# Kernel optimization log

Hardware: AMD Instinct MI355X
Metric: run time of the kernel (lower is better)

The kernel has to match this reference:

```python
import jax, jax.numpy as jnp
import numpy as np

B, S, D, H = 4, 2048, 1024, 16
HD = D // H
FF = 4 * D
EPS = 1e-5


def _layer_norm(x, w, b):
    mu = jnp.mean(x, axis=-1, keepdims=True)
    var = jnp.mean(jnp.square(x - mu), axis=-1, keepdims=True)
    return (x - mu) * jax.lax.rsqrt(var + EPS) * w + b


def setup_inputs() -> dict:
    key = jax.random.key(0)
    ks = jax.random.split(key, 8)
    std = 0.02
    return {
        "x": jax.random.normal(ks[0], (B, S, D), dtype=jnp.float32),
        "ln1_w": jnp.ones((D,), jnp.float32),
        "ln1_b": jnp.zeros((D,), jnp.float32),
        "w_qkv": jax.random.normal(ks[1], (D, 3 * D), dtype=jnp.float32) * std,  # fused QKV, no bias
        "w_proj": jax.random.normal(ks[2], (D, D), dtype=jnp.float32) * std,
        "b_proj": jnp.zeros((D,), jnp.float32),
        "ln2_w": jnp.ones((D,), jnp.float32),
        "ln2_b": jnp.zeros((D,), jnp.float32),
        "w_ff1": jax.random.normal(ks[3], (D, FF), dtype=jnp.float32) * std,
        "b_ff1": jnp.zeros((FF,), jnp.float32),
        "w_ff2": jax.random.normal(ks[4], (FF, D), dtype=jnp.float32) * std,
        "b_ff2": jnp.zeros((D,), jnp.float32),
    }


def reference(x, ln1_w, ln1_b, w_qkv, w_proj, b_proj, ln2_w, ln2_b, w_ff1, b_ff1, w_ff2, b_ff2):
    b, s, d = x.shape
    # --- attention branch (pre-LN) ---
    h = _layer_norm(x, ln1_w, ln1_b)
    kqv = (h @ w_qkv).reshape(b, s, H, HD, 3)  # fused projection, split by last index
    k, q, v = kqv[..., 0], kqv[..., 1], kqv[..., 2]  # each [b, s, H, HD]
    scores = jnp.einsum("bqhd,bkhd->bhqk", q, k) * (HD ** -0.5)  # [b,H,s,s]
    causal = jnp.tril(jnp.ones((s, s), dtype=bool))
    scores = jnp.where(causal, scores, -jnp.inf)
    weights = jax.nn.softmax(scores, axis=-1)
    ctx = jnp.einsum("bhqk,bkhd->bqhd", weights, v).reshape(b, s, d)
    attn_out = ctx @ w_proj + b_proj
    x = x + attn_out
    # --- feed-forward branch (pre-LN) ---
    h = _layer_norm(x, ln2_w, ln2_b)
    ff = jax.nn.gelu(h @ w_ff1 + b_ff1, approximate=False) @ w_ff2 + b_ff2
    return x + ff
```

## Files before the change

kernel.cpp:

```cpp
#include <hip/hip_runtime.h>

typedef unsigned short u16;
typedef unsigned int u32;
typedef __bf16 bf16x8 __attribute__((ext_vector_type(8)));
typedef float f32x4 __attribute__((ext_vector_type(4)));
typedef float f32x16 __attribute__((ext_vector_type(16)));
typedef unsigned short us8 __attribute__((ext_vector_type(8)));
typedef unsigned short us4 __attribute__((ext_vector_type(4)));
typedef unsigned int u32x4 __attribute__((ext_vector_type(4)));

#define B_ 4
#define S_ 2048
#define D_ 1024
#define H_ 16
#define HD_ 64
#define EPS_ 1e-5f
#define SCALE_ (0.125f * 1.44269504088896341f)
#define THR_ 3.0f

__device__ __forceinline__ u16 f2bf(float f) {
  unsigned u = __builtin_bit_cast(unsigned, f);
  u = (u + 0x7FFFu + ((u >> 16) & 1u)) >> 16;
  return (u16)u;
}

__device__ __forceinline__ float gelu_f(float x) {
  float u = x * (2.3022388f + 0.10294971f * x * x);
  float te = __builtin_amdgcn_exp2f(u);
  return x - x * __builtin_amdgcn_rcpf(1.0f + te);
}

typedef const __attribute__((address_space(1))) unsigned int* gp1;
typedef __attribute__((address_space(3))) unsigned int* lp3;
__device__ __forceinline__ void gl_lds16(const void* g, void* l) {
  __builtin_amdgcn_global_load_lds((gp1)(unsigned long long)g,
                                   (lp3)(unsigned int)(unsigned long long)l,
                                   16, 0, 0);
}

__device__ __forceinline__ u32 cvtpk_bf16(float lo, float hi) {
  u32 d;
  asm("v_cvt_pk_bf16_f32 %0, %1, %2" : "=v"(d) : "v"(lo), "v"(hi));
  return d;
}
__device__ __forceinline__ void swap32(u32& a, u32& b) {
  asm("v_permlane32_swap_b32 %0, %1" : "+v"(a), "+v"(b));
}

__device__ __forceinline__ f32x16 zero16() {
  f32x16 z;
#pragma unroll
  for (int i = 0; i < 16; i++) z[i] = 0.f;
  return z;
}

__global__ __launch_bounds__(256) void wconv_kernel(const float* __restrict__ W,
                                                    u16* __restrict__ Wt,
                                                    int Kd, int N) {
  __shared__ u16 tile[32][33];
  int bid = blockIdx.x;
  int nbn = N >> 5;
  int tk = bid / nbn, tn = bid % nbn;
  int tx = threadIdx.x & 31, ty = threadIdx.x >> 5;
#pragma unroll
  for (int i = 0; i < 4; i++) {
    int r = ty + i * 8;
    tile[r][tx] = f2bf(W[(size_t)(tk * 32 + r) * N + tn * 32 + tx]);
  }
  __syncthreads();
#pragma unroll
  for (int i = 0; i < 4; i++) {
    int r = ty + i * 8;
    Wt[(size_t)(tn * 32 + r) * Kd + tk * 32 + tx] = tile[tx][r];
  }
}

__global__ __launch_bounds__(256) void vtrans_kernel(const u16* __restrict__ Vc,
                                                     u16* __restrict__ Vt) {
  __shared__ u16 tile[64][72];
  int bh = blockIdx.x >> 5;
  int sb = blockIdx.x & 31;
  const u16* src = Vc + ((size_t)bh * S_ + sb * 64) * HD_;
  int r = threadIdx.x >> 2, c0 = (threadIdx.x & 3) * 16;
  *(us8*)&tile[r][c0] = *(const us8*)(src + r * HD_ + c0);
  *(us8*)&tile[r][c0 + 8] = *(const us8*)(src + r * HD_ + c0 + 8);
  __syncthreads();
  u16* dst = Vt + (size_t)bh * HD_ * S_ + sb * 64;
  int hd = threadIdx.x >> 2;
  int s0 = (threadIdx.x & 3) * 16;
  us8 a, b;
#pragma unroll
  for (int j = 0; j < 8; j++) a[j] = tile[s0 + j][hd];
#pragma unroll
  for (int j = 0; j < 8; j++) b[j] = tile[s0 + 8 + j][hd];
  *(us8*)(dst + (size_t)hd * S_ + s0) = a;
  *(us8*)(dst + (size_t)hd * S_ + s0 + 8) = b;
}

__global__ __launch_bounds__(256) void ln_kernel(const float* __restrict__ x,
                                                 const float* __restrict__ w,
                                                 const float* __restrict__ b,
                                                 u16* __restrict__ out) {
  int row = blockIdx.x;
  int t = threadIdx.x;
  int lane = t & 63, wid = t >> 6;
  const float4* xr = (const float4*)(x + (size_t)row * D_);
  float4 v = xr[t];
  float s = v.x + v.y + v.z + v.w;
  float q = v.x * v.x + v.y * v.y + v.z * v.z + v.w * v.w;
#pragma unroll
  for (int off = 1; off < 64; off <<= 1) {
    s += __shfl_xor(s, off);
    q += __shfl_xor(q, off);
  }
  __shared__ float red[8];
  if (lane == 0) { red[wid] = s; red[4 + wid] = q; }
  __syncthreads();
  s = red[0] + red[1] + red[2] + red[3];
  q = red[4] + red[5] + red[6] + red[7];
  float mu = s * (1.0f / D_);
  float var = q * (1.0f / D_) - mu * mu;
  float rs = rsqrtf(var + EPS_);
  int c = t * 4;
  float4 wv = *(const float4*)(w + c);
  float4 bv = *(const float4*)(b + c);
  us4 o;
  o[0] = f2bf((v.x - mu) * rs * wv.x + bv.x);
  o[1] = f2bf((v.y - mu) * rs * wv.y + bv.y);
  o[2] = f2bf((v.z - mu) * rs * wv.z + bv.z);
  o[3] = f2bf((v.w - mu) * rs * wv.w + bv.w);
  *(us4*)(out + (size_t)row * D_ + c) = o;
}

template <int MODE>
__global__ __launch_bounds__(256, 3) void gemm_kernel(
    const u16* __restrict__ A, const u16* __restrict__ Bt,
    const float* __restrict__ bias, const float* __restrict__ res,
    float* __restrict__ Cf, u16* __restrict__ Cb,
    u16* __restrict__ Qc, u16* __restrict__ Kc, u16* __restrict__ Vc,
    int M, int N, int K) {
  __shared__ __align__(16) u16 Al[2][128 * 32];
  __shared__ __align__(16) u16 Bl[2][128 * 32];
  int t = threadIdx.x;
  int nbn = N >> 7;
  int nwg = gridDim.x;
  int cpx = nwg >> 3;
  int bid = (blockIdx.x % 8) * cpx + blockIdx.x / 8;
  int bm = bid / nbn, bn = bid % nbn;
  int lane = t & 63, wid = t >> 6;
  int wm = wid >> 1, wn = wid & 1;
  int lrow = lane & 15, lgr = lane >> 4;
  const u16* Ab = A + (size_t)bm * 128 * K;
  const u16* Bb = Bt + (size_t)bn * 128 * K;
  int srow = t >> 2;
  int sslot = (t & 3) ^ (srow & 3);
  const u16* Asrc = Ab + (size_t)srow * K + sslot * 8;
  const u16* Bsrc = Bb + (size_t)srow * K + sslot * 8;
  int rdslot = lgr ^ (lrow & 3);

  f32x4 acc[4][4] = {};
  int NT = K >> 5;
  {
    gl_lds16(Asrc, &Al[0][t * 8]);
    gl_lds16(Asrc + (size_t)64 * K, &Al[0][2048 + t * 8]);
    gl_lds16(Bsrc, &Bl[0][t * 8]);
    gl_lds16(Bsrc + (size_t)64 * K, &Bl[0][2048 + t * 8]);
  }
  for (int kt = 0; kt < NT; kt++) {
    int cur = kt & 1;
    if (kt + 1 < NT) {
      int k1 = (kt + 1) * 32;
      u16* Ad = &Al[cur ^ 1][t * 8];
      u16* Bd = &Bl[cur ^ 1][t * 8];
      gl_lds16(Asrc + k1, Ad);
      gl_lds16(Asrc + (size_t)64 * K + k1, Ad + 2048);
      gl_lds16(Bsrc + k1, Bd);
      gl_lds16(Bsrc + (size_t)64 * K + k1, Bd + 2048);
      asm volatile("s_waitcnt vmcnt(4)" ::: "memory");
    } else {
      asm volatile("s_waitcnt vmcnt(0)" ::: "memory");
    }
    __builtin_amdgcn_sched_barrier(0);
    __builtin_amdgcn_s_barrier();
    __builtin_amdgcn_sched_barrier(0);
    bf16x8 af[4], bfr[4];
#pragma unroll
    for (int m = 0; m < 4; m++)
      af[m] = *(const bf16x8*)&Al[cur][(wm * 64 + m * 16 + lrow) * 32 + rdslot * 8];
#pragma unroll
    for (int n = 0; n < 4; n++)
      bfr[n] = *(const bf16x8*)&Bl[cur][(wn * 64 + n * 16 + lrow) * 32 + rdslot * 8];
    __builtin_amdgcn_s_setprio(1);
#pragma unroll
    for (int m = 0; m < 4; m++)
#pragma unroll
      for (int n = 0; n < 4; n++)
        acc[m][n] = __builtin_amdgcn_mfma_f32_16x16x32_bf16(af[m], bfr[n], acc[m][n], 0, 0, 0);
    __builtin_amdgcn_s_setprio(0);
    __builtin_amdgcn_sched_barrier(0);
    __builtin_amdgcn_s_barrier();
    __builtin_amdgcn_sched_barrier(0);
  }
#pragma unroll
  for (int n = 0; n < 4; n++) {
    int col = bn * 128 + wn * 64 + n * 16 + lrow;
    float bv = (MODE & 1) ? bias[col] : 0.0f;
    if (MODE & 16) {
      int c = col % 3;
      int hd = (col / 3) & 63;
      int h = col / 192;
      u16* dst = (c == 0) ? Kc : (c == 1) ? Qc : Vc;
#pragma unroll
      for (int m = 0; m < 4; m++)
#pragma unroll
        for (int r = 0; r < 4; r++) {
          int row = bm * 128 + wm * 64 + m * 16 + lgr * 4 + r;
          int bb = row >> 11, sIdx = row & 2047;
          dst[(((size_t)(bb * H_ + h)) * S_ + sIdx) * HD_ + hd] = f2bf(acc[m][n][r]);
        }
    } else {
#pragma unroll
      for (int m = 0; m < 4; m++)
#pragma unroll
        for (int r = 0; r < 4; r++) {
          int row = bm * 128 + wm * 64 + m * 16 + lgr * 4 + r;
          float v = acc[m][n][r] + bv;
          if (MODE & 2) v = gelu_f(v);
          if (MODE & 4) v += res[(size_t)row * N + col];
          if (MODE & 8) Cb[(size_t)row * N + col] = f2bf(v);
          else          Cf[(size_t)row * N + col] = v;
        }
    }
  }
}

__device__ __forceinline__ void attn_softmax_update(
    f32x16* s, int NSUB_rt, float& mrun, float& lrun, f32x16 (&o)[2], int hi) {
  float pmax = -3.0e38f;
  for (int sub = 0; sub < NSUB_rt; sub++)
#pragma unroll
    for (int r = 0; r < 16; r++) pmax = fmaxf(pmax, s[sub][r]);
  pmax = fmaxf(pmax, __shfl_xor(pmax, 32));
  bool ok = (pmax * SCALE_ <= mrun + THR_);
  if (!__all(ok)) {
    float mnew = fmaxf(mrun, pmax * SCALE_);
    float corr = __builtin_amdgcn_exp2f(mrun - mnew);
    mrun = mnew;
    lrun *= corr;
#pragma unroll
    for (int r = 0; r < 16; r++) {
      float cr = __shfl(corr, ((r & 3) + 8 * (r >> 2)) + 4 * hi);
      o[0][r] *= cr;
      o[1][r] *= cr;
    }
  }
  float m = mrun;
  float lacc = 0.f;
  for (int sub = 0; sub < NSUB_rt; sub++)
#pragma unroll
    for (int r = 0; r < 16; r++) {
      float p = __builtin_amdgcn_exp2f(__builtin_fmaf(s[sub][r], SCALE_, -m));
      s[sub][r] = p;
      lacc += p;
    }
  lrun += lacc;
}

__device__ __forceinline__ void attn_pfrag(const f32x16& s, bf16x8& pa, bf16x8& pb) {
  u32 a0 = cvtpk_bf16(s[0], s[1]);
  u32 a1 = cvtpk_bf16(s[2], s[3]);
  u32 a2 = cvtpk_bf16(s[4], s[5]);
  u32 a3 = cvtpk_bf16(s[6], s[7]);
  swap32(a0, a2);
  swap32(a1, a3);
  u32 b0 = cvtpk_bf16(s[8], s[9]);
  u32 b1 = cvtpk_bf16(s[10], s[11]);
  u32 b2 = cvtpk_bf16(s[12], s[13]);
  u32 b3 = cvtpk_bf16(s[14], s[15]);
  swap32(b0, b2);
  swap32(b1, b3);
  u32x4 fa = {a0, a1, a2, a3};
  u32x4 fb = {b0, b1, b2, b3};
  pa = __builtin_bit_cast(bf16x8, fa);
  pb = __builtin_bit_cast(bf16x8, fb);
}

template <bool MASK>
__device__ __forceinline__ void attn_chunk_tail(
    const u16* __restrict__ Kh, const u16* __restrict__ Vh,
    const bf16x8 (&qf)[4], f32x16 (&o)[2],
    float& mrun, float& lrun, int kb, int qrow, int hi, int ln31) {
  f32x16 s[1];
  f32x16 z = zero16();
  __builtin_amdgcn_s_setprio(1);
#pragma unroll
  for (int ks = 0; ks < 4; ks++) {
    bf16x8 kfr = *(const bf16x8*)(Kh + (size_t)(kb + ln31) * HD_ + ks * 16 + hi * 8);
    z = __builtin_amdgcn_mfma_f32_32x32x16_bf16(kfr, qf[ks], z, 0, 0, 0);
  }
  __builtin_amdgcn_s_setprio(0);
  if (MASK) {
#pragma unroll
    for (int r = 0; r < 16; r++) {
      int key = kb + (r & 3) + 8 * (r >> 2) + 4 * hi;
      if (key > qrow) z[r] = -3.0e38f;
    }
  }
  s[0] = z;
  attn_softmax_update(s, 1, mrun, lrun, o, hi);
  bf16x8 pa, pb;
  attn_pfrag(s[0], pa, pb);
  __builtin_amdgcn_s_setprio(1);
#pragma unroll
  for (int ht = 0; ht < 2; ht++) {
    const u16* vb = Vh + (size_t)(ht * 32 + ln31) * S_ + kb + hi * 8;
    bf16x8 v1 = *(const bf16x8*)(vb);
    bf16x8 v2 = *(const bf16x8*)(vb + 16);
    o[ht] = __builtin_amdgcn_mfma_f32_32x32x16_bf16(pa, v1, o[ht], 0, 0, 0);
    o[ht] = __builtin_amdgcn_mfma_f32_32x32x16_bf16(pb, v2, o[ht], 0, 0, 0);
  }
  __builtin_amdgcn_s_setprio(0);
}

__global__ __launch_bounds__(512) void attn_kernel(const u16* __restrict__ Q,
                                                   const u16* __restrict__ Kk,
                                                   const u16* __restrict__ Vt,
                                                   u16* __restrict__ ctx) {
  __shared__ __align__(16) u16 Kl[2][64 * 64];
  __shared__ __align__(16) u16 Vl[2][64 * 64];
  int t = threadIdx.x;
  int lane = t & 63, wid = t >> 6;
  int qblk = 7 - (int)(blockIdx.x >> 6);
  int bh = blockIdx.x & 63;
  int b = bh >> 4, h = bh & 15;
  const u16* Qh = Q + (size_t)bh * S_ * HD_;
  const u16* Kh = Kk + (size_t)bh * S_ * HD_;
  const u16* Vh = Vt + (size_t)bh * HD_ * S_;
  int qb = qblk * 256;
  int qbase = qb + wid * 32;
  int ln31 = lane & 31, hi = lane >> 5;
  int qrow = qbase + ln31;
  int l7 = ln31 & 7;

  int srow = t >> 3;
  int sslot = (t & 7) ^ (srow & 7);
  const u16* Ksrc = Kh + (size_t)srow * HD_ + sslot * 8;
  const u16* Vsrc = Vh + (size_t)srow * S_ + sslot * 8;

  bf16x8 qf[4];
#pragma unroll
  for (int ks = 0; ks < 4; ks++)
    qf[ks] = *(const bf16x8*)(Qh + (size_t)qrow * HD_ + ks * 16 + hi * 8);

  f32x16 o[2] = {zero16(), zero16()};
  float mrun = -1.0e30f, lrun = 0.f;

  int nf64 = qbase >> 6;
  int NT = (qb >> 6) + 3;

  gl_lds16(Ksrc, &Kl[0][t * 8]);
  gl_lds16(Vsrc, &Vl[0][t * 8]);
  for (int kt = 0; kt < NT; kt++) {
    int cur = kt & 1;
    if (kt + 1 < NT) {
      int kb1 = (kt + 1) * 64;
      gl_lds16(Ksrc + (size_t)kb1 * HD_, &Kl[cur ^ 1][t * 8]);
      gl_lds16(Vsrc + kb1, &Vl[cur ^ 1][t * 8]);
      asm volatile("s_waitcnt vmcnt(2)" ::: "memory");
    } else {
      asm volatile("s_waitcnt vmcnt(0)" ::: "memory");
    }
    __builtin_amdgcn_sched_barrier(0);
    __builtin_amdgcn_s_barrier();
    __builtin_amdgcn_sched_barrier(0);
    if (kt < nf64) {
      const u16* Kc = &Kl[cur][0];
      const u16* Vc = &Vl[cur][0];
      f32x16 s[2];
#pragma unroll
      for (int sub = 0; sub < 2; sub++) {
        f32x16 z = zero16();
        __builtin_amdgcn_s_setprio(1);
#pragma unroll
        for (int ks = 0; ks < 4; ks++) {
          int kr = sub * 32 + ln31;
          int sl = (ks * 2 + hi) ^ l7;
          bf16x8 kfr = *(const bf16x8*)&Kc[kr * 64 + sl * 8];
          z = __builtin_amdgcn_mfma_f32_32x32x16_bf16(kfr, qf[ks], z, 0, 0, 0);
        }
        __builtin_amdgcn_s_setprio(0);
        s[sub] = z;
      }
      attn_softmax_update(s, 2, mrun, lrun, o, hi);
#pragma unroll
      for (int sub = 0; sub < 2; sub++) {
        bf16x8 pa, pb;
        attn_pfrag(s[sub], pa, pb);
        __builtin_amdgcn_s_setprio(1);
#pragma unroll
        for (int ht = 0; ht < 2; ht++) {
          int vr = ht * 32 + ln31;
          int s1 = (sub * 4 + hi) ^ (vr & 7);
          int s2 = (sub * 4 + hi + 2) ^ (vr & 7);
          bf16x8 v1 = *(const bf16x8*)&Vc[vr * 64 + s1 * 8];
          bf16x8 v2 = *(const bf16x8*)&Vc[vr * 64 + s2 * 8];
          o[ht] = __builtin_amdgcn_mfma_f32_32x32x16_bf16(pa, v1, o[ht], 0, 0, 0);
          o[ht] = __builtin_amdgcn_mfma_f32_32x32x16_bf16(pb, v2, o[ht], 0, 0, 0);
        }
        __builtin_amdgcn_s_setprio(0);
      }
    }
    __builtin_amdgcn_sched_barrier(0);
    __builtin_amdgcn_s_barrier();
    __builtin_amdgcn_sched_barrier(0);
  }

  if (qbase & 32)
    attn_chunk_tail<false>(Kh, Vh, qf, o, mrun, lrun, qbase - 32, qrow, hi, ln31);
  attn_chunk_tail<true>(Kh, Vh, qf, o, mrun, lrun, qbase, qrow, hi, ln31);

  float l = lrun + __shfl_xor(lrun, 32);
  float inv = 1.0f / l;
#pragma unroll
  for (int r = 0; r < 16; r++) {
    float invr = __shfl(inv, ((r & 3) + 8 * (r >> 2)) + 4 * hi);
    int q = qbase + (r & 3) + 8 * (r >> 2) + 4 * hi;
    size_t base = ((size_t)b * S_ + q) * D_ + h * HD_;
    ctx[base + ln31] = f2bf(o[0][r] * invr);
    ctx[base + 32 + ln31] = f2bf(o[1][r] * invr);
  }
}

extern "C" void kernel_launch(void* const* d_in, const int* in_sizes, int n_in,
                              void* d_out, int out_size, void* d_ws, size_t ws_size,
                              hipStream_t stream) {
  const float* x = (const float*)d_in[0];
  const float* ln1w = (const float*)d_in[1];
  const float* ln1b = (const float*)d_in[2];
  const float* wqkv = (const float*)d_in[3];
  const float* wproj = (const float*)d_in[4];
  const float* bproj = (const float*)d_in[5];
  const float* ln2w = (const float*)d_in[6];
  const float* ln2b = (const float*)d_in[7];
  const float* wff1 = (const float*)d_in[8];
  const float* bff1 = (const float*)d_in[9];
  const float* wff2 = (const float*)d_in[10];
  const float* bff2 = (const float*)d_in[11];

  char* ws = (char*)d_ws;
  u16* wqkvT = (u16*)(ws + 0);
  u16* wprojT = (u16*)(ws + 6291456);
  u16* wff1T = (u16*)(ws + 8388608);
  u16* wff2T = (u16*)(ws + 16777216);
  u16* h1 = (u16*)(ws + 25165824);
  u16* Vt = (u16*)(ws + 25165824);
  u16* Qc = (u16*)(ws + 41943040);
  u16* Kc = (u16*)(ws + 58720256);
  u16* Vc = (u16*)(ws + 75497472);
  u16* ctx = (u16*)(ws + 92274688);
  float* x1 = (float*)(ws + 109051904);
  u16* h2 = (u16*)(ws + 142606336);
  u16* g = (u16*)(ws + 25165824);
  float* outp = (float*)d_out;

  wconv_kernel<<<(1024 / 32) * (3072 / 32), 256, 0, stream>>>(wqkv, wqkvT, 1024, 3072);
  wconv_kernel<<<(1024 / 32) * (1024 / 32), 256, 0, stream>>>(wproj, wprojT, 1024, 1024);
  wconv_kernel<<<(1024 / 32) * (4096 / 32), 256, 0, stream>>>(wff1, wff1T, 1024, 4096);
  wconv_kernel<<<(4096 / 32) * (1024 / 32), 256, 0, stream>>>(wff2, wff2T, 4096, 1024);

  ln_kernel<<<8192, 256, 0, stream>>>(x, ln1w, ln1b, h1);
  gemm_kernel<16><<<1536, 256, 0, stream>>>(h1, wqkvT, nullptr, nullptr, nullptr, nullptr,
                                            Qc, Kc, Vc, 8192, 3072, 1024);
  vtrans_kernel<<<64 * 32, 256, 0, stream>>>(Vc, Vt);
  attn_kernel<<<8 * 64, 512, 0, stream>>>(Qc, Kc, Vt, ctx);
  gemm_kernel<5><<<512, 256, 0, stream>>>(ctx, wprojT, bproj, x, x1, nullptr,
                                          nullptr, nullptr, nullptr, 8192, 1024, 1024);
  ln_kernel<<<8192, 256, 0, stream>>>(x1, ln2w, ln2b, h2);
  gemm_kernel<11><<<2048, 256, 0, stream>>>(h2, wff1T, bff1, nullptr, nullptr, g,
                                            nullptr, nullptr, nullptr, 8192, 4096, 1024);
  gemm_kernel<5><<<512, 256, 0, stream>>>(g, wff2T, bff2, x1, outp, nullptr,
                                          nullptr, nullptr, nullptr, 8192, 1024, 4096);
}
```

Baseline: 411.6 us.

## Use single-buffered 64-wide K tiles with supertile block swizzle in GEMM

Rewrites the GEMM main loop to stage 128x64 K-slices in a single LDS buffer per operand, with an 8-way XOR swizzle, instead of double-buffered 128x32 slices. This halves the number of barrier pairs per K. Blocks are remapped into 8x8 supertiles of output tiles to improve L2 reuse. It also drops the occupancy hint of 3 in launch bounds. The trade-off is that global loads no longer overlap MFMA work within a block, so hiding latency depends on other resident blocks.

Result: faster. 370.4 us (-10.0%).

```diff
diff --git a/kernel.cpp b/kernel.cpp
--- a/kernel.cpp
+++ b/kernel.cpp
@@ -133,73 +133,71 @@
 }
 
 template <int MODE>
-__global__ __launch_bounds__(256, 3) void gemm_kernel(
+__global__ __launch_bounds__(256) void gemm_kernel(
     const u16* __restrict__ A, const u16* __restrict__ Bt,
     const float* __restrict__ bias, const float* __restrict__ res,
     float* __restrict__ Cf, u16* __restrict__ Cb,
     u16* __restrict__ Qc, u16* __restrict__ Kc, u16* __restrict__ Vc,
     int M, int N, int K) {
-  __shared__ __align__(16) u16 Al[2][128 * 32];
-  __shared__ __align__(16) u16 Bl[2][128 * 32];
+  __shared__ __align__(16) u16 Al[128 * 64];
+  __shared__ __align__(16) u16 Bl[128 * 64];
   int t = threadIdx.x;
   int nbn = N >> 7;
-  int nwg = gridDim.x;
-  int cpx = nwg >> 3;
-  int bid = (blockIdx.x % 8) * cpx + blockIdx.x / 8;
-  int bm = bid / nbn, bn = bid % nbn;
+  int nwg = gridDim.x, cpx = nwg >> 3;
+  int bid = (blockIdx.x & 7) * cpx + (blockIdx.x >> 3);
+  int nsn = nbn >> 3;
+  int st = bid >> 6, u = bid & 63;
+  int bm = (st / nsn) * 8 + (u >> 3);
+  int bn = (st % nsn) * 8 + (u & 7);
   int lane = t & 63, wid = t >> 6;
   int wm = wid >> 1, wn = wid & 1;
   int lrow = lane & 15, lgr = lane >> 4;
+  int sl7 = lrow & 7;
   const u16* Ab = A + (size_t)bm * 128 * K;
   const u16* Bb = Bt + (size_t)bn * 128 * K;
-  int srow = t >> 2;
-  int sslot = (t & 3) ^ (srow & 3);
-  const u16* Asrc = Ab + (size_t)srow * K + sslot * 8;
-  const u16* Bsrc = Bb + (size_t)srow * K + sslot * 8;
-  int rdslot = lgr ^ (lrow & 3);
-
+  int sr = lane >> 3;
+  int sc = ((lane & 7) ^ sr) << 3;
+  const u16* Ag[4];
+  const u16* Bg[4];
+  u16* Ald[4];
+  u16* Bld[4];
+#pragma unroll
+  for (int j = 0; j < 4; j++) {
+    int row0 = (j * 4 + wid) * 8;
+    Ag[j] = Ab + (size_t)(row0 + sr) * K + sc;
+    Bg[j] = Bb + (size_t)(row0 + sr) * K + sc;
+    Ald[j] = &Al[row0 * 64 + lane * 8];
+    Bld[j] = &Bl[row0 * 64 + lane * 8];
+  }
   f32x4 acc[4][4] = {};
-  int NT = K >> 5;
-  {
-    gl_lds16(Asrc, &Al[0][t * 8]);
-    gl_lds16(Asrc + (size_t)64 * K, &Al[0][2048 + t * 8]);
-    gl_lds16(Bsrc, &Bl[0][t * 8]);
-    gl_lds16(Bsrc + (size_t)64 * K, &Bl[0][2048 + t * 8]);
-  }
-  for (int kt = 0; kt < NT; kt++) {
-    int cur = kt & 1;
-    if (kt + 1 < NT) {
-      int k1 = (kt + 1) * 32;
-      u16* Ad = &Al[cur ^ 1][t * 8];
-      u16* Bd = &Bl[cur ^ 1][t * 8];
-      gl_lds16(Asrc + k1, Ad);
-      gl_lds16(Asrc + (size_t)64 * K + k1, Ad + 2048);
-      gl_lds16(Bsrc + k1, Bd);
-      gl_lds16(Bsrc + (size_t)64 * K + k1, Bd + 2048);
-      asm volatile("s_waitcnt vmcnt(4)" ::: "memory");
-    } else {
-      asm volatile("s_waitcnt vmcnt(0)" ::: "memory");
-    }
-    __builtin_amdgcn_sched_barrier(0);
-    __builtin_amdgcn_s_barrier();
-    __builtin_amdgcn_sched_barrier(0);
-    bf16x8 af[4], bfr[4];
+  for (int k0 = 0; k0 < K; k0 += 64) {
+#pragma unroll
+    for (int j = 0; j < 4; j++) {
+      gl_lds16(Ag[j] + k0, Ald[j]);
+      gl_lds16(Bg[j] + k0, Bld[j]);
+    }
+    __syncthreads();
+    bf16x8 af[2][4], bfr[2][4];
+#pragma unroll
+    for (int ks = 0; ks < 2; ks++) {
+      int slot = ((ks << 2) | lgr) ^ sl7;
+#pragma unroll
+      for (int m = 0; m < 4; m++)
+        af[ks][m] = *(const bf16x8*)&Al[(wm * 64 + m * 16 + lrow) * 64 + slot * 8];
+#pragma unroll
+      for (int n = 0; n < 4; n++)
+        bfr[ks][n] = *(const bf16x8*)&Bl[(wn * 64 + n * 16 + lrow) * 64 + slot * 8];
+    }
+    __builtin_amdgcn_s_setprio(1);
 #pragma unroll
     for (int m = 0; m < 4; m++)
-      af[m] = *(const bf16x8*)&Al[cur][(wm * 64 + m * 16 + lrow) * 32 + rdslot * 8];
-#pragma unroll
-    for (int n = 0; n < 4; n++)
-      bfr[n] = *(const bf16x8*)&Bl[cur][(wn * 64 + n * 16 + lrow) * 32 + rdslot * 8];
-    __builtin_amdgcn_s_setprio(1);
-#pragma unroll
-    for (int m = 0; m < 4; m++)
-#pragma unroll
-      for (int n = 0; n < 4; n++)
-        acc[m][n] = __builtin_amdgcn_mfma_f32_16x16x32_bf16(af[m], bfr[n], acc[m][n], 0, 0, 0);
+#pragma unroll
+      for (int n = 0; n < 4; n++) {
+        acc[m][n] = __builtin_amdgcn_mfma_f32_16x16x32_bf16(af[0][m], bfr[0][n], acc[m][n], 0, 0, 0);
+        acc[m][n] = __builtin_amdgcn_mfma_f32_16x16x32_bf16(af[1][m], bfr[1][n], acc[m][n], 0, 0, 0);
+      }
     __builtin_amdgcn_s_setprio(0);
-    __builtin_amdgcn_sched_barrier(0);
-    __builtin_amdgcn_s_barrier();
-    __builtin_amdgcn_sched_barrier(0);
+    __syncthreads();
   }
 #pragma unroll
   for (int n = 0; n < 4; n++) {
```
